# Optimization experiments

Hardware: AMD Instinct MI355X
Metric: run time of the kernel (lower is better)

Reference implementation:

```python
import jax, jax.numpy as jnp
import numpy as np


def setup_inputs() -> dict:
    key = jax.random.key(0)
    k1, k2 = jax.random.split(key)
    B, S, H, D = 2, 2048, 16, 64
    qk = jax.random.normal(k1, (B, S, 2, H, D), dtype=jnp.float32)
    v = jax.random.normal(k2, (B, S, H, D), dtype=jnp.float32)
    return {"qk": qk, "v": v}


def reference(qk, v):
    # qk: (B, S, 2, H, D); v: (B, S, H, D)
    seqlen = qk.shape[1]
    q = qk[:, :, 0]  # (B, S, H, D)
    k = qk[:, :, 1]
    # elu(x) + 1 feature map (positive features)
    q = jax.nn.elu(q) + 1.0
    k = jax.nn.elu(k) + 1.0
    # explicit O(S^2) score matrix: (B, H, T, S)
    scores = jnp.einsum('bthd,bshd->bhts', q, k)
    mask = jnp.tril(jnp.ones((seqlen, seqlen), dtype=scores.dtype))
    scores = scores * mask
    nu = scores.sum(axis=-1)  # (B, H, T)
    attention = scores / nu[:, :, :, None]
    # dropout_p = 0.0 (eval mode): identity
    output = jnp.einsum('bhts,bshd->bthd', attention, v)
    return output
```

## Files before the change

### kernel.cpp

```cpp
#include <hip/hip_runtime.h>


#define BB 2
#define SS 2048
#define HH 16
#define DD 64
#define CC 128
#define NC (SS / CC)
#define BH (BB * HH)
#define NCHUNK (BH * NC)

#define ST_STRIDE 8448LL
#define WS_KB (512LL * ST_STRIDE)
#define WS_VT (WS_KB + 512LL * 16384)

typedef __attribute__((ext_vector_type(8))) short bf16x8;
typedef __attribute__((ext_vector_type(4))) float f32x4;

__device__ __forceinline__ float phi(float x) {
    return x > 0.f ? x + 1.f : __expf(x);
}
__device__ __forceinline__ unsigned short f2bf(float x) {
    unsigned int u = __float_as_uint(x);
    u += 0x7fffu + ((u >> 16) & 1u);
    return (unsigned short)(u >> 16);
}
__device__ __forceinline__ float bf2f(unsigned short b) {
    return __uint_as_float(((unsigned int)b) << 16);
}
__device__ __forceinline__ void gload16(const void* g, void* lds) {
    __builtin_amdgcn_global_load_lds(
        (const __attribute__((address_space(1))) unsigned int*)g,
        (__attribute__((address_space(3))) unsigned int*)lds, 16, 0, 0);
}

__global__ __launch_bounds__(256, 2)
void prep_state(const float* __restrict__ qk, const float* __restrict__ v,
                char* __restrict__ st, unsigned short* __restrict__ kbg,
                unsigned short* __restrict__ vtg) {
    __shared__ unsigned short Kt[DD][136];
    __shared__ unsigned short Vt[DD][136];

    const int tid = threadIdx.x, blk = blockIdx.x;
    const int bh = blk / NC, c = blk % NC, b = bh / HH, h = bh % HH;
    const int s0 = c * CC;
    const int lr = tid >> 4, lc = (tid & 15) * 4;
    char* kbc = (char*)kbg + (size_t)blk * 16384;

    #pragma unroll
    for (int it = 0; it < 8; ++it) {
        int row = it * 16 + lr;
        size_t ka = ((size_t)((b * SS + s0 + row) * 2 + 1)) * (HH * DD) + h * DD + lc;
        float4 kv = *(const float4*)(qk + ka);
        ushort4 kq = make_ushort4(f2bf(phi(kv.x)), f2bf(phi(kv.y)),
                                  f2bf(phi(kv.z)), f2bf(phi(kv.w)));
        *(ushort4*)(kbc + row * 128 + ((lc * 2) ^ ((row & 7) << 4))) = kq;
        Kt[lc + 0][row] = kq.x; Kt[lc + 1][row] = kq.y;
        Kt[lc + 2][row] = kq.z; Kt[lc + 3][row] = kq.w;
        size_t va = ((size_t)((b * SS + s0 + row) * HH + h)) * DD + lc;
        float4 vv = *(const float4*)(v + va);
        Vt[lc + 0][row] = f2bf(vv.x); Vt[lc + 1][row] = f2bf(vv.y);
        Vt[lc + 2][row] = f2bf(vv.z); Vt[lc + 3][row] = f2bf(vv.w);
    }
    __syncthreads();

    {
        char* vtc = (char*)vtg + (size_t)blk * 16384;
        int e = tid >> 2, sq = (tid & 3) * 32;
        #pragma unroll
        for (int k8 = 0; k8 < 4; ++k8) {
            int s = sq + k8 * 8;
            bf16x8 val = *(const bf16x8*)&Vt[e][s];
            *(bf16x8*)(vtc + e * 256 + ((s * 2) ^ ((e & 7) << 4))) = val;
        }
    }

    const int w = tid >> 6, lane = tid & 63, g = lane >> 4, ln = lane & 15;
    {
        bf16x8 av[4];
        #pragma unroll
        for (int ks = 0; ks < 4; ++ks)
            av[ks] = *(const bf16x8*)&Vt[w * 16 + ln][ks * 32 + g * 8];
        bf16x8 ones;
        #pragma unroll
        for (int j = 0; j < 8; ++j) ones[j] = (short)0x3F80;

        char* stc = st + (size_t)blk * ST_STRIDE;
        #pragma unroll
        for (int n = 0; n < 4; ++n) {
            f32x4 a = {0.f, 0.f, 0.f, 0.f}, kz4 = {0.f, 0.f, 0.f, 0.f};
            #pragma unroll
            for (int ks = 0; ks < 4; ++ks) {
                bf16x8 bk = *(const bf16x8*)&Kt[n * 16 + ln][ks * 32 + g * 8];
                a = __builtin_amdgcn_mfma_f32_16x16x32_bf16(av[ks], bk, a, 0, 0, 0);
                if (w == 0)
                    kz4 = __builtin_amdgcn_mfma_f32_16x16x32_bf16(ones, bk, kz4, 0, 0, 0);
            }
            #pragma unroll
            for (int r = 0; r < 4; ++r)
                *(unsigned short*)(stc + (((w * 16 + g * 4 + r) * 64) + n * 16 + ln) * 2)
                    = f2bf(a[r]);
            if (w == 0 && g == 0)
                *(float*)(stc + 8192 + (n * 16 + ln) * 4) = kz4[0];
        }
    }
}

__global__ __launch_bounds__(256, 2)
void lin_attn_out(const float* __restrict__ qk,
                  const unsigned short* __restrict__ kbg,
                  const unsigned short* __restrict__ vtg,
                  const char* __restrict__ st,
                  float* __restrict__ out) {
    __shared__ __align__(16) char KbL[16384];
    __shared__ __align__(16) char VtL[16384];
    __shared__ __align__(16) char S0L[8192];
    __shared__ float kzl[DD];
    __shared__ float nul[4][32];

    const int tid = threadIdx.x, blk = blockIdx.x;
    const int bh = blk / NC, c = blk % NC, b = bh / HH, h = bh % HH;
    const int s0 = c * CC;
    const int w = tid >> 6, lane = tid & 63, g = lane >> 4, ln = lane & 15;
    const int wband = (blk & 1) ? (3 - w) : w;

    {
        const char* kbs = (const char*)kbg + (size_t)blk * 16384;
        const char* vts = (const char*)vtg + (size_t)blk * 16384;
        #pragma unroll
        for (int i = 0; i < 4; ++i) {
            gload16(kbs + w * 4096 + i * 1024 + lane * 16, KbL + w * 4096 + i * 1024);
            gload16(vts + w * 4096 + i * 1024 + lane * 16, VtL + w * 4096 + i * 1024);
        }
    }

    {
        const char* stb = st + (size_t)(bh * NC) * ST_STRIDE;
        float acc[16];
        #pragma unroll
        for (int j = 0; j < 16; ++j) acc[j] = 0.f;
        for (int c2 = 0; c2 < c; ++c2) {
            const char* src = stb + (size_t)c2 * ST_STRIDE + tid * 32;
            bf16x8 x0 = *(const bf16x8*)src;
            bf16x8 x1 = *(const bf16x8*)(src + 16);
            #pragma unroll
            for (int j = 0; j < 8; ++j) {
                acc[j]     += bf2f((unsigned short)x0[j]);
                acc[j + 8] += bf2f((unsigned short)x1[j]);
            }
        }
        int e = tid >> 2, d0 = (tid & 3) * 16;
        bf16x8 o0, o1;
        #pragma unroll
        for (int j = 0; j < 8; ++j) {
            o0[j] = (short)f2bf(acc[j]);
            o1[j] = (short)f2bf(acc[j + 8]);
        }
        int sw = (e & 7) << 4;
        *(bf16x8*)(S0L + e * 128 + ((2 * d0) ^ sw)) = o0;
        *(bf16x8*)(S0L + e * 128 + ((2 * d0 + 16) ^ sw)) = o1;
        if (tid < DD) {
            float a = 0.f;
            for (int c2 = 0; c2 < c; ++c2)
                a += *(const float*)(stb + (size_t)c2 * ST_STRIDE + 8192 + 4 * tid);
            kzl[tid] = a;
        }
    }

    bf16x8 aq[2][2];
    #pragma unroll
    for (int m = 0; m < 2; ++m) {
        int tg = s0 + wband * 32 + m * 16 + ln;
        const float* qrow = qk + ((size_t)((b * SS + tg) * 2)) * (HH * DD) + h * DD;
        #pragma unroll
        for (int kb2 = 0; kb2 < 2; ++kb2) {
            float4 x0 = *(const float4*)(qrow + kb2 * 32 + g * 8);
            float4 x1 = *(const float4*)(qrow + kb2 * 32 + g * 8 + 4);
            bf16x8 f;
            f[0] = (short)f2bf(phi(x0.x)); f[1] = (short)f2bf(phi(x0.y));
            f[2] = (short)f2bf(phi(x0.z)); f[3] = (short)f2bf(phi(x0.w));
            f[4] = (short)f2bf(phi(x1.x)); f[5] = (short)f2bf(phi(x1.y));
            f[6] = (short)f2bf(phi(x1.z)); f[7] = (short)f2bf(phi(x1.w));
            aq[m][kb2] = f;
        }
    }
    __syncthreads();

    f32x4 O[2][4];
    #pragma unroll
    for (int m = 0; m < 2; ++m)
        #pragma unroll
        for (int n = 0; n < 4; ++n) O[m][n] = (f32x4){0.f, 0.f, 0.f, 0.f};

    #pragma unroll
    for (int n = 0; n < 4; ++n) {
        int e = n * 16 + ln;
        bf16x8 b0 = *(const bf16x8*)(S0L + e * 128 + ((g * 16) ^ ((e & 7) << 4)));
        bf16x8 b1 = *(const bf16x8*)(S0L + e * 128 + ((64 + g * 16) ^ ((e & 7) << 4)));
        #pragma unroll
        for (int m = 0; m < 2; ++m) {
            O[m][n] = __builtin_amdgcn_mfma_f32_16x16x32_bf16(aq[m][0], b0, O[m][n], 0, 0, 0);
            O[m][n] = __builtin_amdgcn_mfma_f32_16x16x32_bf16(aq[m][1], b1, O[m][n], 0, 0, 0);
        }
    }

    float nuA[2] = {0.f, 0.f};
    #pragma unroll
    for (int kb2 = 0; kb2 < 2; ++kb2)
        #pragma unroll
        for (int j = 0; j < 8; ++j) {
            float kzv = kzl[kb2 * 32 + g * 8 + j];
            nuA[0] = fmaf(bf2f((unsigned short)aq[0][kb2][j]), kzv, nuA[0]);
            nuA[1] = fmaf(bf2f((unsigned short)aq[1][kb2][j]), kzv, nuA[1]);
        }

    const int srcA = ((lane & 16) << 1) + ln;
    const bool hiT = (lane & 32) != 0;
    for (int sblk = 0; sblk <= wband; ++sblk) {
        const bool diag = (sblk == wband);
        f32x4 ScT[2][2];
        #pragma unroll
        for (int m = 0; m < 2; ++m)
            #pragma unroll
            for (int ns = 0; ns < 2; ++ns) ScT[m][ns] = (f32x4){0.f, 0.f, 0.f, 0.f};

        #pragma unroll
        for (int ns = 0; ns < 2; ++ns) {
            int s = sblk * 32 + ns * 16 + ln;
            const char* srow = KbL + s * 128;
            bf16x8 bk0 = *(const bf16x8*)(srow + ((g * 16) ^ ((s & 7) << 4)));
            bf16x8 bk1 = *(const bf16x8*)(srow + ((64 + g * 16) ^ ((s & 7) << 4)));
            #pragma unroll
            for (int m = 0; m < 2; ++m) {
                ScT[m][ns] = __builtin_amdgcn_mfma_f32_16x16x32_bf16(bk0, aq[m][0], ScT[m][ns], 0, 0, 0);
                ScT[m][ns] = __builtin_amdgcn_mfma_f32_16x16x32_bf16(bk1, aq[m][1], ScT[m][ns], 0, 0, 0);
            }
        }

        #pragma unroll
        for (int m = 0; m < 2; ++m)
            #pragma unroll
            for (int ns = 0; ns < 2; ++ns)
                #pragma unroll
                for (int r = 0; r < 4; ++r) {
                    if (diag && (ns * 16 + g * 4 + r > m * 16 + ln))
                        ScT[m][ns][r] = 0.f;
                    nuA[m] += ScT[m][ns][r];
                }

        bf16x8 bv[4];
        #pragma unroll
        for (int n = 0; n < 4; ++n) {
            int e = n * 16 + ln;
            bv[n] = *(const bf16x8*)(VtL + e * 256 + ((sblk * 64 + g * 16) ^ ((e & 7) << 4)));
        }

        #pragma unroll
        for (int m = 0; m < 2; ++m) {
            bf16x8 pa;
            #pragma unroll
            for (int j = 0; j < 8; ++j) {
                int sl = (j < 4) ? srcA : (srcA + 16);
                float v0 = __shfl(ScT[m][0][j & 3], sl);
                float v1 = __shfl(ScT[m][1][j & 3], sl);
                pa[j] = (short)f2bf(hiT ? v1 : v0);
            }
            #pragma unroll
            for (int n = 0; n < 4; ++n)
                O[m][n] = __builtin_amdgcn_mfma_f32_16x16x32_bf16(pa, bv[n], O[m][n], 0, 0, 0);
        }
    }

    #pragma unroll
    for (int m = 0; m < 2; ++m) {
        float nt = nuA[m];
        nt += __shfl_xor(nt, 16);
        nt += __shfl_xor(nt, 32);
        if (g == 0) nul[w][m * 16 + ln] = nt;
    }
    asm volatile("s_waitcnt lgkmcnt(0)" ::: "memory");
    __builtin_amdgcn_sched_barrier(0);

    #pragma unroll
    for (int m = 0; m < 2; ++m) {
        float inv[4];
        #pragma unroll
        for (int r = 0; r < 4; ++r) inv[r] = 1.f / nul[w][m * 16 + g * 4 + r];
        #pragma unroll
        for (int n = 0; n < 4; ++n)
            #pragma unroll
            for (int r = 0; r < 4; ++r) {
                int t = wband * 32 + m * 16 + g * 4 + r;
                int e = n * 16 + ln;
                size_t oa = ((size_t)((b * SS + s0 + t) * HH + h)) * DD + e;
                out[oa] = O[m][n][r] * inv[r];
            }
    }
}

extern "C" void kernel_launch(void* const* d_in, const int* in_sizes, int n_in,
                              void* d_out, int out_size, void* d_ws, size_t ws_size,
                              hipStream_t stream) {
    const float* qk = (const float*)d_in[0];
    const float* v  = (const float*)d_in[1];
    float* outp = (float*)d_out;

    char* st = (char*)d_ws;
    unsigned short* kbg = (unsigned short*)((char*)d_ws + WS_KB);
    unsigned short* vtg = (unsigned short*)((char*)d_ws + WS_VT);

    prep_state<<<NCHUNK, 256, 0, stream>>>(qk, v, st, kbg, vtg);
    lin_attn_out<<<NCHUNK, 256, 0, stream>>>(qk, kbg, vtg, st, outp);
}
```

Measured before the change: 37.56 us.

## Stage score tiles through LDS, swizzle block order, split state-prefix reductions

Score tiles are now computed non-transposed and written as bf16 into a per-wave LDS buffer. They are read back as MFMA A operands, replacing the 16 cross-lane shuffles per tile. The row-sum normaliser is taken from the rounded bf16 values, which slightly changes numerics. Block indices are remapped with an XOR-style swizzle so neighbouring blocks span different heads and chunks. The prefix-sum of earlier chunk states uses two accumulator chains, and the kz reduction is spread over all threads with shuffles instead of 64 serial threads. prep_state's launch bound rises to 4 blocks per SM. The extra LDS buffer and wait add latency per tile.

```diff
diff --git a/kernel.cpp b/kernel.cpp
--- a/kernel.cpp
+++ b/kernel.cpp
@@ -33,15 +33,18 @@
         (const __attribute__((address_space(1))) unsigned int*)g,
         (__attribute__((address_space(3))) unsigned int*)lds, 16, 0, 0);
 }
-
-__global__ __launch_bounds__(256, 2)
+__device__ __forceinline__ int xswz(int hw) {
+    return ((hw & 7) << 6) | (hw >> 3);
+}
+
+__global__ __launch_bounds__(256, 4)
 void prep_state(const float* __restrict__ qk, const float* __restrict__ v,
                 char* __restrict__ st, unsigned short* __restrict__ kbg,
                 unsigned short* __restrict__ vtg) {
     __shared__ unsigned short Kt[DD][136];
     __shared__ unsigned short Vt[DD][136];
 
-    const int tid = threadIdx.x, blk = blockIdx.x;
+    const int tid = threadIdx.x, blk = xswz(blockIdx.x);
     const int bh = blk / NC, c = blk % NC, b = bh / HH, h = bh % HH;
     const int s0 = c * CC;
     const int lr = tid >> 4, lc = (tid & 15) * 4;
@@ -116,13 +119,14 @@
     __shared__ __align__(16) char VtL[16384];
     __shared__ __align__(16) char S0L[8192];
     __shared__ float kzl[DD];
+    __shared__ __align__(16) unsigned short Wl[4][32][40];
     __shared__ float nul[4][32];
 
-    const int tid = threadIdx.x, blk = blockIdx.x;
+    const int tid = threadIdx.x, blk = xswz(blockIdx.x);
     const int bh = blk / NC, c = blk % NC, b = bh / HH, h = bh % HH;
     const int s0 = c * CC;
     const int w = tid >> 6, lane = tid & 63, g = lane >> 4, ln = lane & 15;
-    const int wband = (blk & 1) ? (3 - w) : w;
+    const int wband = ((blk >> 5) & 1) ? (3 - w) : w;
 
     {
         const char* kbs = (const char*)kbg + (size_t)blk * 16384;
@@ -135,36 +139,52 @@
     }
 
     {
-        const char* stb = st + (size_t)(bh * NC) * ST_STRIDE;
-        float acc[16];
-        #pragma unroll
-        for (int j = 0; j < 16; ++j) acc[j] = 0.f;
-        for (int c2 = 0; c2 < c; ++c2) {
-            const char* src = stb + (size_t)c2 * ST_STRIDE + tid * 32;
-            bf16x8 x0 = *(const bf16x8*)src;
-            bf16x8 x1 = *(const bf16x8*)(src + 16);
+        const char* stb = st + (size_t)bh * NC * ST_STRIDE;
+        const char* src = stb + tid * 32;
+        float accA[16], accB[16];
+        #pragma unroll
+        for (int j = 0; j < 16; ++j) { accA[j] = 0.f; accB[j] = 0.f; }
+        int c2 = 0;
+        for (; c2 + 2 <= c; c2 += 2) {
+            bf16x8 xa0 = *(const bf16x8*)(src + (size_t)c2 * ST_STRIDE);
+            bf16x8 xa1 = *(const bf16x8*)(src + (size_t)c2 * ST_STRIDE + 16);
+            bf16x8 xb0 = *(const bf16x8*)(src + (size_t)(c2 + 1) * ST_STRIDE);
+            bf16x8 xb1 = *(const bf16x8*)(src + (size_t)(c2 + 1) * ST_STRIDE + 16);
             #pragma unroll
             for (int j = 0; j < 8; ++j) {
-                acc[j]     += bf2f((unsigned short)x0[j]);
-                acc[j + 8] += bf2f((unsigned short)x1[j]);
+                accA[j]     += bf2f((unsigned short)xa0[j]);
+                accA[j + 8] += bf2f((unsigned short)xa1[j]);
+                accB[j]     += bf2f((unsigned short)xb0[j]);
+                accB[j + 8] += bf2f((unsigned short)xb1[j]);
+            }
+        }
+        if (c2 < c) {
+            bf16x8 xa0 = *(const bf16x8*)(src + (size_t)c2 * ST_STRIDE);
+            bf16x8 xa1 = *(const bf16x8*)(src + (size_t)c2 * ST_STRIDE + 16);
+            #pragma unroll
+            for (int j = 0; j < 8; ++j) {
+                accA[j]     += bf2f((unsigned short)xa0[j]);
+                accA[j + 8] += bf2f((unsigned short)xa1[j]);
             }
         }
         int e = tid >> 2, d0 = (tid & 3) * 16;
         bf16x8 o0, o1;
         #pragma unroll
         for (int j = 0; j < 8; ++j) {
-            o0[j] = (short)f2bf(acc[j]);
-            o1[j] = (short)f2bf(acc[j + 8]);
+            o0[j] = (short)f2bf(accA[j] + accB[j]);
+            o1[j] = (short)f2bf(accA[j + 8] + accB[j + 8]);
         }
         int sw = (e & 7) << 4;
         *(bf16x8*)(S0L + e * 128 + ((2 * d0) ^ sw)) = o0;
         *(bf16x8*)(S0L + e * 128 + ((2 * d0 + 16) ^ sw)) = o1;
-        if (tid < DD) {
-            float a = 0.f;
-            for (int c2 = 0; c2 < c; ++c2)
-                a += *(const float*)(stb + (size_t)c2 * ST_STRIDE + 8192 + 4 * tid);
-            kzl[tid] = a;
-        }
+
+        int chain = tid & 3;
+        float a = 0.f;
+        for (int cc = chain; cc < c; cc += 4)
+            a += *(const float*)(stb + (size_t)cc * ST_STRIDE + 8192 + 4 * e);
+        a += __shfl_xor(a, 1);
+        a += __shfl_xor(a, 2);
+        if (chain == 0) kzl[e] = a;
     }
 
     bf16x8 aq[2][2];
@@ -214,15 +234,13 @@
             nuA[1] = fmaf(bf2f((unsigned short)aq[1][kb2][j]), kzv, nuA[1]);
         }
 
-    const int srcA = ((lane & 16) << 1) + ln;
-    const bool hiT = (lane & 32) != 0;
     for (int sblk = 0; sblk <= wband; ++sblk) {
         const bool diag = (sblk == wband);
-        f32x4 ScT[2][2];
+        f32x4 Sc[2][2];
         #pragma unroll
         for (int m = 0; m < 2; ++m)
             #pragma unroll
-            for (int ns = 0; ns < 2; ++ns) ScT[m][ns] = (f32x4){0.f, 0.f, 0.f, 0.f};
+            for (int ns = 0; ns < 2; ++ns) Sc[m][ns] = (f32x4){0.f, 0.f, 0.f, 0.f};
 
         #pragma unroll
         for (int ns = 0; ns < 2; ++ns) {
@@ -232,8 +250,8 @@
             bf16x8 bk1 = *(const bf16x8*)(srow + ((64 + g * 16) ^ ((s & 7) << 4)));
             #pragma unroll
             for (int m = 0; m < 2; ++m) {
-                ScT[m][ns] = __builtin_amdgcn_mfma_f32_16x16x32_bf16(bk0, aq[m][0], ScT[m][ns], 0, 0, 0);
-                ScT[m][ns] = __builtin_amdgcn_mfma_f32_16x16x32_bf16(bk1, aq[m][1], ScT[m][ns], 0, 0, 0);
+                Sc[m][ns] = __builtin_amdgcn_mfma_f32_16x16x32_bf16(aq[m][0], bk0, Sc[m][ns], 0, 0, 0);
+                Sc[m][ns] = __builtin_amdgcn_mfma_f32_16x16x32_bf16(aq[m][1], bk1, Sc[m][ns], 0, 0, 0);
             }
         }
 
@@ -243,10 +261,14 @@
             for (int ns = 0; ns < 2; ++ns)
                 #pragma unroll
                 for (int r = 0; r < 4; ++r) {
-                    if (diag && (ns * 16 + g * 4 + r > m * 16 + ln))
-                        ScT[m][ns][r] = 0.f;
-                    nuA[m] += ScT[m][ns][r];
+                    int t_loc = m * 16 + g * 4 + r;
+                    int s_loc = ns * 16 + ln;
+                    float val = Sc[m][ns][r];
+                    if (diag && s_loc > t_loc) val = 0.f;
+                    Wl[w][t_loc][s_loc] = f2bf(val);
                 }
+        asm volatile("s_waitcnt lgkmcnt(0)" ::: "memory");
+        __builtin_amdgcn_sched_barrier(0);
 
         bf16x8 bv[4];
         #pragma unroll
@@ -257,14 +279,11 @@
 
         #pragma unroll
         for (int m = 0; m < 2; ++m) {
-            bf16x8 pa;
-            #pragma unroll
-            for (int j = 0; j < 8; ++j) {
-                int sl = (j < 4) ? srcA : (srcA + 16);
-                float v0 = __shfl(ScT[m][0][j & 3], sl);
-                float v1 = __shfl(ScT[m][1][j & 3], sl);
-                pa[j] = (short)f2bf(hiT ? v1 : v0);
-            }
+            bf16x8 pa = *(const bf16x8*)&Wl[w][m * 16 + ln][g * 8];
+            float rs = 0.f;
+            #pragma unroll
+            for (int j = 0; j < 8; ++j) rs += bf2f((unsigned short)pa[j]);
+            nuA[m] += rs;
             #pragma unroll
             for (int n = 0; n < 4; ++n)
                 O[m][n] = __builtin_amdgcn_mfma_f32_16x16x32_bf16(pa, bv[n], O[m][n], 0, 0, 0);
```

Result: faster. 36.39 us (-3.1%).
